# Kernel tuning notes

Measured on AMD Instinct MI355X. Metric: run time of the kernel, lower is better.

Reference implementation:

```python
import jax, jax.numpy as jnp
import numpy as np

N_NODES = 100000
N_EDGES = 1600000
NEG_SLOPE = 0.2
EPS = 1e-6


def setup_inputs() -> dict:
    key = jax.random.key(0)
    ks = jax.random.split(key, 14)
    s = 0.1  # weight init scale
    return {
        "x": jax.random.normal(ks[0], (N_NODES, 64), jnp.float32),
        "src": jax.random.randint(ks[1], (N_EDGES,), 0, N_NODES, jnp.int32),
        "dst": jax.random.randint(ks[2], (N_EDGES,), 0, N_NODES, jnp.int32),
        "W0": s * jax.random.normal(ks[3], (64, 128), jnp.float32),
        "al0": s * jax.random.normal(ks[4], (4, 32), jnp.float32),
        "ar0": s * jax.random.normal(ks[5], (4, 32), jnp.float32),
        "W1": s * jax.random.normal(ks[6], (128, 128), jnp.float32),
        "al1": s * jax.random.normal(ks[7], (4, 32), jnp.float32),
        "ar1": s * jax.random.normal(ks[8], (4, 32), jnp.float32),
        "resW1": s * jax.random.normal(ks[9], (128, 128), jnp.float32),
        "W2": s * jax.random.normal(ks[10], (128, 32), jnp.float32),
        "al2": s * jax.random.normal(ks[11], (1, 32), jnp.float32),
        "ar2": s * jax.random.normal(ks[12], (1, 32), jnp.float32),
        "resW2": s * jax.random.normal(ks[13], (128, 32), jnp.float32),
    }


def gat_conv(h, src, dst, W, al, ar, resW):
    """DGL-style GATConv. h: [N, Fin]; returns [N, H, D]."""
    H, D = al.shape
    feat = (h @ W).reshape(-1, H, D)                       # [N,H,D]
    el = jnp.sum(feat * al, axis=-1)                       # [N,H]
    er = jnp.sum(feat * ar, axis=-1)                       # [N,H]
    e = jax.nn.leaky_relu(el[src] + er[dst], NEG_SLOPE)    # [E,H]
    # segment softmax over destination nodes
    m = jax.ops.segment_max(e, dst, num_segments=N_NODES)  # [N,H]
    ex = jnp.exp(e - m[dst])                               # [E,H]
    denom = jax.ops.segment_sum(ex, dst, num_segments=N_NODES)
    alpha = ex / denom[dst]                                # [E,H]
    msg = alpha[:, :, None] * feat[src]                    # [E,H,D]
    rst = jax.ops.segment_sum(msg, dst, num_segments=N_NODES)  # [N,H,D]
    if resW is not None:
        rst = rst + (h @ resW).reshape(-1, H, D)
    return rst


def pairnorm_scs(x, scale=1.0):
    # 'PN-SCS' mode: scale-individually then center by original column mean
    col_mean = jnp.mean(x, axis=0)
    rownorm = jnp.sqrt(EPS + jnp.sum(x * x, axis=1, keepdims=True))
    return scale * x / rownorm - col_mean


def reference(x, src, dst, W0, al0, ar0, W1, al1, ar1, resW1, W2, al2, ar2, resW2):
    # layer 0: no residual, activation applied outside
    h = gat_conv(x, src, dst, W0, al0, ar0, None)          # [N,4,32]
    h = jax.nn.elu(h.reshape(h.shape[0], -1))              # [N,128]
    h = pairnorm_scs(h)
    # middle layer: residual + internal ELU (DGL applies activation inside),
    # then the outer loop flattens and applies ELU again
    h = jax.nn.elu(gat_conv(h, src, dst, W1, al1, ar1, resW1))  # [N,4,32]
    h = jax.nn.elu(h.reshape(h.shape[0], -1))              # [N,128]
    h = pairnorm_scs(h)
    # final layer: residual, mean over heads
    h = gat_conv(h, src, dst, W2, al2, ar2, resW2)         # [N,1,32]
    h = jnp.mean(h, axis=1)                                # [N,32]
    # dgl.mean_nodes readout on a single graph -> mean over nodes
    return jnp.mean(h, axis=0)                             # [32]
```

## Files before the change

### kernel.cpp

```cpp
#include <hip/hip_runtime.h>


typedef __attribute__((ext_vector_type(8))) short s8v;
typedef __attribute__((ext_vector_type(4))) float f4v;
typedef __attribute__((ext_vector_type(2))) float f2v;
typedef __attribute__((ext_vector_type(2))) _Float16 h2;
typedef __attribute__((ext_vector_type(4))) _Float16 h4;

__device__ __forceinline__ unsigned short f2bf(float f) {
  unsigned int x = __float_as_uint(f);
  x += 0x7fffu + ((x >> 16) & 1u);
  return (unsigned short)(x >> 16);
}
__device__ __forceinline__ float bf2f(unsigned short u) {
  return __uint_as_float(((unsigned int)u) << 16);
}
__device__ __forceinline__ unsigned short f2h(float f) {
  _Float16 h = (_Float16)f;
  return __builtin_bit_cast(unsigned short, h);
}
__device__ __forceinline__ unsigned char f2fp8(float v) {
  return (unsigned char)(__builtin_amdgcn_cvt_pk_fp8_f32(v, v, 0, false) & 0xff);
}
__device__ __forceinline__ float lrelu(float x) { return fmaxf(x, 0.2f * x); }
__device__ __forceinline__ float elu1(float x) { return x > 0.f ? x : __expf(x) - 1.f; }

__device__ __forceinline__ void pack_one(const float* W, const float* al, const float* ar,
                                         const float* resW, unsigned short* out,
                                         int K, int M, int BF, int H, int RES0, int t) {
  int c = t / K, k = t - c * K;
  float v = 0.f;
  if (c < BF) {
    v = W[k * BF + c];
  } else if (c < BF + H) {
    int h = c - BF;
    float s = 0.f;
    for (int d = 0; d < 32; d++) s += W[k * BF + h * 32 + d] * al[h * 32 + d];
    v = s;
  } else if (c < BF + 2 * H) {
    int h = c - BF - H;
    float s = 0.f;
    for (int d = 0; d < 32; d++) s += W[k * BF + h * 32 + d] * ar[h * 32 + d];
    v = s;
  } else if (c >= RES0) {
    v = resW[k * (M - RES0) + (c - RES0)];
  }
  unsigned short hi = f2bf(v);
  out[c * K + k] = hi;
  out[M * K + c * K + k] = f2bf(v - bf2f(hi));
}

__global__ __launch_bounds__(256) void hist_pack_k(const int* __restrict__ dst,
                                                   int* __restrict__ bhist, int E, int NB, int chunk, int P2B,
                                                   const float* __restrict__ W0, const float* __restrict__ al0,
                                                   const float* __restrict__ ar0,
                                                   const float* __restrict__ W1, const float* __restrict__ al1,
                                                   const float* __restrict__ ar1, const float* __restrict__ resW1,
                                                   const float* __restrict__ W2, const float* __restrict__ al2,
                                                   const float* __restrict__ ar2, const float* __restrict__ resW2,
                                                   unsigned short* __restrict__ w0t, unsigned short* __restrict__ w1t,
                                                   unsigned short* __restrict__ w2t) {
  if ((int)blockIdx.x < P2B) {
    __shared__ int h[512];
    for (int b = threadIdx.x; b < NB; b += 256) h[b] = 0;
    __syncthreads();
    int e0 = blockIdx.x * chunk;
    int e1 = min(E, e0 + chunk);
    for (int e = e0 + threadIdx.x; e < e1; e += 256) atomicAdd(&h[dst[e] >> 8], 1);
    __syncthreads();
    for (int b = threadIdx.x; b < NB; b += 256)
      bhist[(size_t)b * P2B + blockIdx.x] = h[b];
  } else {
    const int n0 = 144 * 64, n1 = 272 * 128, n2 = 80 * 128;
    int t = ((int)blockIdx.x - P2B) * 256 + threadIdx.x;
    if (t < n0) {
      pack_one(W0, al0, ar0, nullptr, w0t, 64, 144, 128, 4, 144, t);
    } else if (t < n0 + n1) {
      pack_one(W1, al1, ar1, resW1, w1t, 128, 272, 128, 4, 144, t - n0);
    } else if (t < n0 + n1 + n2) {
      pack_one(W2, al2, ar2, resW2, w2t, 128, 80, 32, 1, 48, t - n0 - n1);
    }
  }
}

__global__ __launch_bounds__(256) void pscan1(int* __restrict__ arr, int* __restrict__ bsum, int Nn) {
  __shared__ int s[256];
  int t = threadIdx.x;
  int base = blockIdx.x * 1024 + t * 4;
  int v0 = (base + 0 < Nn) ? arr[base + 0] : 0;
  int v1 = (base + 1 < Nn) ? arr[base + 1] : 0;
  int v2 = (base + 2 < Nn) ? arr[base + 2] : 0;
  int v3 = (base + 3 < Nn) ? arr[base + 3] : 0;
  s[t] = v0 + v1 + v2 + v3;
  __syncthreads();
  for (int off = 1; off < 256; off <<= 1) {
    int xv = (t >= off) ? s[t - off] : 0;
    __syncthreads();
    s[t] += xv;
    __syncthreads();
  }
  int excl = t ? s[t - 1] : 0;
  if (t == 255) bsum[blockIdx.x] = s[255];
  if (base + 0 < Nn) { arr[base + 0] = excl; excl += v0; }
  if (base + 1 < Nn) { arr[base + 1] = excl; excl += v1; }
  if (base + 2 < Nn) { arr[base + 2] = excl; excl += v2; }
  if (base + 3 < Nn) { arr[base + 3] = excl; }
}

__global__ __launch_bounds__(256) void pscan2(int* __restrict__ arr, const int* __restrict__ bsum,
                                              int Nn, int nb) {
  __shared__ int s[256];
  int t = threadIdx.x;
  s[t] = (t < nb) ? bsum[t] : 0;
  __syncthreads();
  for (int off = 1; off < 256; off <<= 1) {
    int xv = (t >= off) ? s[t - off] : 0;
    __syncthreads();
    s[t] += xv;
    __syncthreads();
  }
  int bb = blockIdx.x;
  int pref = bb ? s[bb - 1] : 0;
  if (pref != 0) {
    int base = bb * 1024 + t * 4;
    if (base + 0 < Nn) arr[base + 0] += pref;
    if (base + 1 < Nn) arr[base + 1] += pref;
    if (base + 2 < Nn) arr[base + 2] += pref;
    if (base + 3 < Nn) arr[base + 3] += pref;
  }
}

__global__ __launch_bounds__(256) void bscatter_k(const int* __restrict__ src, const int* __restrict__ dst,
                                                  const int* __restrict__ seg, unsigned int* __restrict__ ebuf,
                                                  int E, int NB, int chunk) {
  __shared__ int cur[512];
  for (int b = threadIdx.x; b < NB; b += 256)
    cur[b] = seg[(size_t)b * gridDim.x + blockIdx.x];
  __syncthreads();
  int e0 = blockIdx.x * chunk;
  int e1 = min(E, e0 + chunk);
  for (int e = e0 + threadIdx.x; e < e1; e += 256) {
    int d = dst[e];
    int pos = atomicAdd(&cur[d >> 8], 1);
    ebuf[pos] = ((unsigned int)src[e] << 8) | (unsigned int)(d & 255);
  }
}

__global__ __launch_bounds__(256) void fscatter_k(const unsigned int* __restrict__ ebuf,
                                                  const int* __restrict__ seg,
                                                  int* __restrict__ csr_src,
                                                  int* __restrict__ counts, int* __restrict__ rsp,
                                                  int E, int NB, int P2B, int Nn) {
  __shared__ int cnt[256];
  __shared__ int sc[256];
  __shared__ int cur[256];
  int b = blockIdx.x;
  int t = threadIdx.x;
  cnt[t] = 0;
  __syncthreads();
  int bstart = seg[(size_t)b * P2B];
  int bend = (b + 1 < NB) ? seg[(size_t)(b + 1) * P2B] : E;
  for (int e = bstart + t; e < bend; e += 256)
    atomicAdd(&cnt[ebuf[e] & 255u], 1);
  __syncthreads();
  int v = cnt[t];
  sc[t] = v;
  __syncthreads();
  for (int off = 1; off < 256; off <<= 1) {
    int xv = (t >= off) ? sc[t - off] : 0;
    __syncthreads();
    sc[t] += xv;
    __syncthreads();
  }
  int base = bstart + (t ? sc[t - 1] : 0);
  int node = (b << 8) + t;
  if (node < Nn) { counts[node] = v; rsp[node] = base; }
  cur[t] = base;
  __syncthreads();
  for (int e = bstart + t; e < bend; e += 256) {
    unsigned int sd = ebuf[e];
    int pos = atomicAdd(&cur[sd & 255u], 1);
    csr_src[pos] = (int)(sd >> 8);
  }
}

__global__ __launch_bounds__(256) void cmw_k(const float* __restrict__ colsum,
                                             const unsigned short* __restrict__ wt,
                                             float* __restrict__ cmw, int K, int M, float invN) {
  int c = blockIdx.x * 256 + threadIdx.x;
  if (c >= M) return;
  float s = 0.f;
  for (int k = 0; k < K; k++)
    s += colsum[k] * (bf2f(wt[c * K + k]) + bf2f(wt[(size_t)M * K + c * K + k]));
  cmw[c] = s * invN;
}

template <int K, int M, int R, int BF, int H, int RES0, bool AF32, bool CMW>
__global__ __launch_bounds__(256) void gemm_bf16(const void* __restrict__ Av,
                                                 const unsigned short* __restrict__ Bt,
                                                 const float* __restrict__ cmw,
                                                 unsigned char* __restrict__ feat8,
                                                 float* __restrict__ el, float* __restrict__ er,
                                                 unsigned short* __restrict__ resh, int nRowTiles) {
  constexpr int NT = M / 16;
  constexpr int PLANE = 16 * K * 2;
  constexpr int RS = (K == 128) ? 8 : 7;
  __shared__ unsigned char bbuf[2 * PLANE];
  int t = threadIdx.x;
  int w = t >> 6;
  int lane = t & 63;
  int tile0 = (int)blockIdx.x * (4 * R) + w * R;
  int r = lane & 15, q = lane >> 4;

  s8v afrag[R][K / 32];
  bool valid[R];
#pragma unroll
  for (int rr = 0; rr < R; rr++) {
    valid[rr] = (tile0 + rr) < nRowTiles;
    if (valid[rr]) {
      if constexpr (AF32) {
        const float* arow = (const float*)Av + (size_t)((tile0 + rr) * 16 + r) * K + q * 8;
#pragma unroll
        for (int kk = 0; kk < K / 32; kk++) {
          s8v v;
#pragma unroll
          for (int j = 0; j < 8; j++) v[j] = (short)f2bf(arow[kk * 32 + j]);
          afrag[rr][kk] = v;
        }
      } else {
        const unsigned short* arow = (const unsigned short*)Av + (size_t)((tile0 + rr) * 16 + r) * K + q * 8;
#pragma unroll
        for (int kk = 0; kk < K / 32; kk++) afrag[rr][kk] = *(const s8v*)(arow + kk * 32);
      }
    }
  }

  const unsigned char* gBhi = (const unsigned char*)Bt;
  const unsigned char* gBlo = (const unsigned char*)Bt + (size_t)M * K * 2;

  uint4 rh = {0, 0, 0, 0}, rl = {0, 0, 0, 0};
  if constexpr (K == 128) {
    rh = *(const uint4*)(gBhi + (size_t)0 * PLANE + t * 16);
    rl = *(const uint4*)(gBlo + (size_t)0 * PLANE + t * 16);
  } else {
    if (t < 128) rh = *(const uint4*)(gBhi + t * 16);
    else         rl = *(const uint4*)(gBlo + (t - 128) * 16);
  }

  for (int ct = 0; ct < NT; ct++) {
    if constexpr (K == 128) {
      unsigned x = (unsigned)t * 16;
      unsigned d = x ^ (((x >> RS) & 7u) << 4);
      *(uint4*)(bbuf + d) = rh;
      *(uint4*)(bbuf + PLANE + d) = rl;
    } else {
      if (t < 128) {
        unsigned x = (unsigned)t * 16;
        unsigned d = x ^ (((x >> RS) & 7u) << 4);
        *(uint4*)(bbuf + d) = rh;
      } else {
        unsigned x = (unsigned)(t - 128) * 16;
        unsigned d = x ^ (((x >> RS) & 7u) << 4);
        *(uint4*)(bbuf + PLANE + d) = rl;
      }
    }
    __syncthreads();
    if (ct + 1 < NT) {
      if constexpr (K == 128) {
        rh = *(const uint4*)(gBhi + (size_t)(ct + 1) * PLANE + t * 16);
        rl = *(const uint4*)(gBlo + (size_t)(ct + 1) * PLANE + t * 16);
      } else {
        if (t < 128) rh = *(const uint4*)(gBhi + (size_t)(ct + 1) * PLANE + t * 16);
        else         rl = *(const uint4*)(gBlo + (size_t)(ct + 1) * PLANE + (t - 128) * 16);
      }
    }
    s8v bhi[K / 32], blo[K / 32];
#pragma unroll
    for (int kk = 0; kk < K / 32; kk++) {
      unsigned off = (unsigned)(q * 16 + kk * 64);
      unsigned ad = ((unsigned)r << RS) + (off ^ (((unsigned)(r & 7)) << 4));
      bhi[kk] = *(const s8v*)(bbuf + ad);
      blo[kk] = *(const s8v*)(bbuf + PLANE + ad);
    }
    int col = ct * 16 + r;
    float cmwv = 0.f;
    if constexpr (CMW) cmwv = cmw[col];
#pragma unroll
    for (int rr = 0; rr < R; rr++) {
      if (!valid[rr]) continue;
      f4v acc = {0.f, 0.f, 0.f, 0.f};
#pragma unroll
      for (int kk = 0; kk < K / 32; kk++) {
        acc = __builtin_amdgcn_mfma_f32_16x16x32_bf16(afrag[rr][kk], bhi[kk], acc, 0, 0, 0);
        acc = __builtin_amdgcn_mfma_f32_16x16x32_bf16(afrag[rr][kk], blo[kk], acc, 0, 0, 0);
      }
      int row0 = (tile0 + rr) * 16 + q * 4;
#pragma unroll
      for (int i = 0; i < 4; i++) {
        float v = acc[i] - cmwv;
        size_t row = (size_t)(row0 + i);
        if (col < BF) {
          feat8[row * BF + col] = f2fp8(v);
        } else if (col < BF + H) {
          el[row * H + (col - BF)] = v;
        } else if (col < BF + 2 * H) {
          er[row * H + (col - BF - H)] = v;
        } else if (RES0 < M && col >= RES0) {
          resh[row * (M - RES0) + (col - RES0)] = f2h(v);
        }
      }
    }
    __syncthreads();
  }
}

template <int MODE>
__global__ __launch_bounds__(256) void aggregate4(const unsigned char* __restrict__ feat8,
                                                  const float* __restrict__ el4,
                                                  const float* __restrict__ er4,
                                                  const int* __restrict__ csr_src,
                                                  const int* __restrict__ rsp,
                                                  const int* __restrict__ counts,
                                                  const unsigned short* __restrict__ resh,
                                                  unsigned short* __restrict__ vbf,
                                                  float* __restrict__ rnrm, int Nn) {
  int n = (int)((blockIdx.x * blockDim.x + threadIdx.x) >> 6);
  if (n >= Nn) return;
  int lane = threadIdx.x & 63;
  int start = __builtin_amdgcn_readfirstlane(rsp[n]);
  int deg = __builtin_amdgcn_readfirstlane(counts[n]);
  int chunks = (deg + 15) >> 4;
  int slot = lane >> 2, h = lane & 3;
  float ern = er4[(size_t)n * 4 + h];
  int hl = lane >> 4;
  unsigned dby = (unsigned)lane << 1;
  f2v a01 = {0.f, 0.f};
  float dsum = 0.f;
  float elv = el4[(size_t)csr_src[start + slot] * 4 + h];
  for (int c = 0; c < chunks; c++) {
    const int* csp = csr_src + start + (c << 4);
    int sj[16];
#pragma unroll
    for (int j = 0; j < 16; j++) sj[j] = csp[j];
    float e = elv + ern;
    float exv = (((c << 4) + slot) < deg) ? __expf(fmaxf(e, 0.2f * e)) : 0.f;
    dsum += exv;
    if (c + 1 < chunks) elv = el4[(size_t)csp[16 + slot] * 4 + h];
#pragma unroll
    for (int j = 0; j < 16; j++) {
      float aw = __shfl(exv, (j << 2) | hl);
      unsigned short u = *(const unsigned short*)(feat8 + (((unsigned)sj[j] << 7) + dby));
      f2v fv = __builtin_amdgcn_cvt_pk_f32_fp8((int)u, false);
      f2v aw2 = {aw, aw};
      a01 = __builtin_elementwise_fma(fv, aw2, a01);
    }
  }
#pragma unroll
  for (int off = 4; off < 64; off <<= 1) dsum += __shfl_xor(dsum, off);
  float inv = dsum > 0.f ? 1.f / dsum : 0.f;
  float invh = __shfl(inv, hl);
  float v0, v1;
  if (MODE == 1) {
    h2 rr = *(const h2*)(resh + (size_t)n * 128 + lane * 2);
    v0 = elu1(elu1(a01[0] * invh + (float)rr[0]));
    v1 = elu1(elu1(a01[1] * invh + (float)rr[1]));
  } else {
    v0 = elu1(a01[0] * invh);
    v1 = elu1(a01[1] * invh);
  }
  float ss = v0 * v0 + v1 * v1;
#pragma unroll
  for (int off = 1; off < 64; off <<= 1) ss += __shfl_xor(ss, off);
  float rn = sqrtf(1e-6f + ss);
  float ri = 1.f / rn;
  unsigned int pk = (unsigned int)f2bf(v0 * ri) | ((unsigned int)f2bf(v1 * ri) << 16);
  *(unsigned int*)((char*)vbf + ((size_t)n << 8) + (lane << 2)) = pk;
  if (lane == 0) rnrm[n] = rn;
}

__global__ __launch_bounds__(256) void aggregate1(const unsigned char* __restrict__ feat8,
                                                  const float* __restrict__ el1,
                                                  const float* __restrict__ er1,
                                                  const int* __restrict__ csr_src,
                                                  const int* __restrict__ rsp,
                                                  const int* __restrict__ counts,
                                                  const unsigned short* __restrict__ res2h,
                                                  float* __restrict__ out2, int Nn) {
  int n = (int)((blockIdx.x * blockDim.x + threadIdx.x) >> 6);
  if (n >= Nn) return;
  int lane = threadIdx.x & 63;
  int start = __builtin_amdgcn_readfirstlane(rsp[n]);
  int deg = __builtin_amdgcn_readfirstlane(counts[n]);
  int chunks = (deg + 15) >> 4;
  int l16 = lane & 15;
  float ern = er1[n];
  int g = lane >> 3;
  unsigned dofs4 = (unsigned)(lane & 7) << 2;
  f2v acc01 = {0.f, 0.f}, acc23 = {0.f, 0.f};
  float dsum = 0.f;
  int sA = csr_src[start + l16];
  float elv = el1[sA];
  for (int c = 0; c < chunks; c++) {
    const int* csp = csr_src + start + (c << 4);
    float exv = (((c << 4) + l16) < deg) ? __expf(lrelu(elv + ern)) : 0.f;
    dsum += exv;
    int sAc = sA;
    if (c + 1 < chunks) {
      sA = csp[16 + l16];
      elv = el1[sA];
    }
#pragma unroll
    for (int t = 0; t < 2; t++) {
      int j = (t << 3) + g;
      int sj = __shfl(sAc, j);
      float aw = __shfl(exv, j);
      f2v aw2 = {aw, aw};
      unsigned int u = *(const unsigned int*)(feat8 + (((unsigned)sj << 5) + dofs4));
      f2v fa = __builtin_amdgcn_cvt_pk_f32_fp8((int)u, false);
      f2v fb = __builtin_amdgcn_cvt_pk_f32_fp8((int)u, true);
      acc01 = __builtin_elementwise_fma(fa, aw2, acc01);
      acc23 = __builtin_elementwise_fma(fb, aw2, acc23);
    }
  }
#pragma unroll
  for (int off = 1; off < 16; off <<= 1) dsum += __shfl_xor(dsum, off);
  float inv = dsum > 0.f ? 1.f / dsum : 0.f;
#pragma unroll
  for (int off = 8; off < 64; off <<= 1) {
    acc01[0] += __shfl_xor(acc01[0], off);
    acc01[1] += __shfl_xor(acc01[1], off);
    acc23[0] += __shfl_xor(acc23[0], off);
    acc23[1] += __shfl_xor(acc23[1], off);
  }
  if (lane < 8) {
    h4 rr = *(const h4*)(res2h + (size_t)n * 32 + (lane << 2));
    float4 o;
    o.x = acc01[0] * inv + (float)rr[0];
    o.y = acc01[1] * inv + (float)rr[1];
    o.z = acc23[0] * inv + (float)rr[2];
    o.w = acc23[1] * inv + (float)rr[3];
    *(float4*)(out2 + (size_t)n * 32 + (lane << 2)) = o;
  }
}

__global__ __launch_bounds__(256) void colsum_k(const unsigned short* __restrict__ vbf,
                                                const float* __restrict__ rnrm,
                                                float* __restrict__ colsum, int Nn) {
  __shared__ float ls[256];
  int tid = threadIdx.x;
  int c = tid & 127, rsub = tid >> 7;
  float cs = 0.f;
  for (int r = blockIdx.x * 2 + rsub; r < Nn; r += gridDim.x * 2)
    cs += bf2f(vbf[(size_t)r * 128 + c]) * rnrm[r];
  ls[tid] = cs;
  __syncthreads();
  if (tid < 128) atomicAdd(&colsum[tid], ls[tid] + ls[tid + 128]);
}

__global__ __launch_bounds__(256) void final_reduce(const float* __restrict__ out2,
                                                    float* __restrict__ outsum, int Nn) {
  __shared__ float ls[32];
  if (threadIdx.x < 32) ls[threadIdx.x] = 0.f;
  __syncthreads();
  int d = threadIdx.x & 31, rl = threadIdx.x >> 5;
  float acc = 0.f;
  for (int n = blockIdx.x * 8 + rl; n < Nn; n += gridDim.x * 8)
    acc += out2[(size_t)n * 32 + d];
  atomicAdd(&ls[d], acc);
  __syncthreads();
  if (threadIdx.x < 32) atomicAdd(&outsum[threadIdx.x], ls[threadIdx.x]);
}

__global__ void finalize_k(const float* __restrict__ outsum, float* __restrict__ out, float invN) {
  int t = threadIdx.x;
  if (t < 32) out[t] = outsum[t] * invN;
}

extern "C" void kernel_launch(void* const* d_in, const int* in_sizes, int n_in,
                              void* d_out, int out_size, void* d_ws, size_t ws_size,
                              hipStream_t stream) {
  const float* x     = (const float*)d_in[0];
  const int*   src   = (const int*)d_in[1];
  const int*   dst   = (const int*)d_in[2];
  const float* W0    = (const float*)d_in[3];
  const float* al0   = (const float*)d_in[4];
  const float* ar0   = (const float*)d_in[5];
  const float* W1    = (const float*)d_in[6];
  const float* al1   = (const float*)d_in[7];
  const float* ar1   = (const float*)d_in[8];
  const float* resW1 = (const float*)d_in[9];
  const float* W2    = (const float*)d_in[10];
  const float* al2   = (const float*)d_in[11];
  const float* ar2   = (const float*)d_in[12];
  const float* resW2 = (const float*)d_in[13];
  const int N = in_sizes[0] / 64;
  const int E = in_sizes[1];
  const float invN = 1.f / (float)N;
  const int Emax = E + 64;
  const int NB = (N + 255) >> 8;
  const int P2B = 512;
  const int chunk = (E + P2B - 1) / P2B;
  const int segN = NB * P2B;
  const int nbB = (segN + 1023) / 1024;

  char* p = (char*)d_ws;
  auto alloc = [&](size_t bytes) { char* r = p; p += (bytes + 255) & ~(size_t)255; return r; };

  char* zbase = p;
  float* colsumA = (float*)alloc(512);
  float* colsumB = (float*)alloc(512);
  float* outsum  = (float*)alloc(128);
  size_t zbytes = (size_t)(p - zbase);

  int* counts = (int*)alloc((size_t)4 * N);
  int* rsp    = (int*)alloc((size_t)4 * N);
  int* bsumB  = (int*)alloc(1024);
  int* bhist  = (int*)alloc((size_t)4 * segN);
  unsigned int* ebuf = (unsigned int*)alloc((size_t)4 * E);
  int* csr_src = (int*)alloc((size_t)4 * Emax);
  unsigned char*  feat8 = (unsigned char*)alloc((size_t)N * 128);
  unsigned short* vbf   = (unsigned short*)alloc((size_t)2 * N * 128);
  unsigned short* resh  = (unsigned short*)alloc((size_t)2 * N * 128);
  unsigned short* w0t = (unsigned short*)alloc((size_t)2 * 2 * 144 * 64);
  unsigned short* w1t = (unsigned short*)alloc((size_t)2 * 2 * 272 * 128);
  unsigned short* w2t = (unsigned short*)alloc((size_t)2 * 2 * 80 * 128);
  float* el4  = (float*)alloc((size_t)16 * N);
  float* er4  = (float*)alloc((size_t)16 * N);
  float* rnrm = (float*)alloc((size_t)4 * N);
  float* cmw1 = (float*)alloc(4 * 272);
  float* cmw2 = (float*)alloc(4 * 80);
  float* out2 = (float*)alloc((size_t)4 * N * 32);

  hipMemsetAsync(zbase, 0, zbytes, stream);
  hipMemsetAsync(csr_src + E, 0, (size_t)4 * (Emax - E), stream);

  const int packTot = 144 * 64 + 272 * 128 + 80 * 128;
  const int packBlocks = (packTot + 255) / 256;
  hist_pack_k<<<P2B + packBlocks, 256, 0, stream>>>(dst, bhist, E, NB, chunk, P2B,
                                                    W0, al0, ar0, W1, al1, ar1, resW1,
                                                    W2, al2, ar2, resW2, w0t, w1t, w2t);
  pscan1<<<nbB, 256, 0, stream>>>(bhist, bsumB, segN);
  pscan2<<<nbB, 256, 0, stream>>>(bhist, bsumB, segN, nbB);
  bscatter_k<<<P2B, 256, 0, stream>>>(src, dst, bhist, ebuf, E, NB, chunk);
  fscatter_k<<<NB, 256, 0, stream>>>(ebuf, bhist, csr_src, counts, rsp, E, NB, P2B, N);

  const int rowTiles = N / 16;
  const int gblocks = (rowTiles + 7) / 8;
  const int aggblocks = (N + 3) / 4;

  gemm_bf16<64, 144, 2, 128, 4, 144, true, false><<<gblocks, 256, 0, stream>>>(
      x, w0t, nullptr, feat8, el4, er4, nullptr, rowTiles);
  aggregate4<0><<<aggblocks, 256, 0, stream>>>(feat8, el4, er4, csr_src, rsp, counts, nullptr, vbf, rnrm, N);
  colsum_k<<<512, 256, 0, stream>>>(vbf, rnrm, colsumA, N);
  cmw_k<<<2, 256, 0, stream>>>(colsumA, w1t, cmw1, 128, 272, invN);

  gemm_bf16<128, 272, 2, 128, 4, 144, false, true><<<gblocks, 256, 0, stream>>>(
      vbf, w1t, cmw1, feat8, el4, er4, resh, rowTiles);
  aggregate4<1><<<aggblocks, 256, 0, stream>>>(feat8, el4, er4, csr_src, rsp, counts, resh, vbf, rnrm, N);
  colsum_k<<<512, 256, 0, stream>>>(vbf, rnrm, colsumB, N);
  cmw_k<<<1, 256, 0, stream>>>(colsumB, w2t, cmw2, 128, 80, invN);

  gemm_bf16<128, 80, 2, 32, 1, 48, false, true><<<gblocks, 256, 0, stream>>>(
      vbf, w2t, cmw2, feat8, el4, er4, resh, rowTiles);
  aggregate1<<<aggblocks, 256, 0, stream>>>(feat8, el4, er4, csr_src, rsp, counts, resh, out2, N);
  final_reduce<<<512, 256, 0, stream>>>(out2, outsum, N);
  finalize_k<<<1, 64, 0, stream>>>(outsum, (float*)d_out, invN);
}
```

Before: 488.8 us.

## Fuse scan fixup into scatter kernels, vectorize edge loads, prefetch CSR indices

Removes the pscan2 launch by having bscatter_k and fscatter_k each rescan the block sums in shared memory and add the prefix on the fly. The histogram and scatter kernels now read dst/src as int4 with the chunk size rounded to a multiple of four. The aggregation kernel software-prefetches the next chunk's CSR source indices into registers, and colsum reads two bf16 columns per thread. Together these aim to cut launch overhead and raise memory-access width, at the cost of redundant per-block scans and extra register pressure in the aggregation kernel.

```diff
diff --git a/kernel.cpp b/kernel.cpp
--- a/kernel.cpp
+++ b/kernel.cpp
@@ -66,7 +66,15 @@
     __syncthreads();
     int e0 = blockIdx.x * chunk;
     int e1 = min(E, e0 + chunk);
-    for (int e = e0 + threadIdx.x; e < e1; e += 256) atomicAdd(&h[dst[e] >> 8], 1);
+    int e = e0 + threadIdx.x * 4;
+    for (; e + 3 < e1; e += 1024) {
+      int4 d4 = *(const int4*)(dst + e);
+      atomicAdd(&h[d4.x >> 8], 1);
+      atomicAdd(&h[d4.y >> 8], 1);
+      atomicAdd(&h[d4.z >> 8], 1);
+      atomicAdd(&h[d4.w >> 8], 1);
+    }
+    for (; e < e1; e++) atomicAdd(&h[dst[e] >> 8], 1);
     __syncthreads();
     for (int b = threadIdx.x; b < NB; b += 256)
       bhist[(size_t)b * P2B + blockIdx.x] = h[b];
@@ -107,39 +115,43 @@
   if (base + 3 < Nn) { arr[base + 3] = excl; }
 }
 
-__global__ __launch_bounds__(256) void pscan2(int* __restrict__ arr, const int* __restrict__ bsum,
-                                              int Nn, int nb) {
-  __shared__ int s[256];
+__global__ __launch_bounds__(256) void bscatter_k(const int* __restrict__ src, const int* __restrict__ dst,
+                                                  const int* __restrict__ bhist, const int* __restrict__ bsumB,
+                                                  unsigned int* __restrict__ ebuf,
+                                                  int E, int NB, int chunk, int nbB) {
+  __shared__ int pref[256];
+  __shared__ int cur[512];
   int t = threadIdx.x;
-  s[t] = (t < nb) ? bsum[t] : 0;
+  pref[t] = (t < nbB) ? bsumB[t] : 0;
   __syncthreads();
   for (int off = 1; off < 256; off <<= 1) {
-    int xv = (t >= off) ? s[t - off] : 0;
-    __syncthreads();
-    s[t] += xv;
-    __syncthreads();
-  }
-  int bb = blockIdx.x;
-  int pref = bb ? s[bb - 1] : 0;
-  if (pref != 0) {
-    int base = bb * 1024 + t * 4;
-    if (base + 0 < Nn) arr[base + 0] += pref;
-    if (base + 1 < Nn) arr[base + 1] += pref;
-    if (base + 2 < Nn) arr[base + 2] += pref;
-    if (base + 3 < Nn) arr[base + 3] += pref;
-  }
-}
-
-__global__ __launch_bounds__(256) void bscatter_k(const int* __restrict__ src, const int* __restrict__ dst,
-                                                  const int* __restrict__ seg, unsigned int* __restrict__ ebuf,
-                                                  int E, int NB, int chunk) {
-  __shared__ int cur[512];
-  for (int b = threadIdx.x; b < NB; b += 256)
-    cur[b] = seg[(size_t)b * gridDim.x + blockIdx.x];
+    int xv = (t >= off) ? pref[t - off] : 0;
+    __syncthreads();
+    pref[t] += xv;
+    __syncthreads();
+  }
+  for (int b = t; b < NB; b += 256) {
+    size_t idx = (size_t)b * gridDim.x + blockIdx.x;
+    int sb = (int)(idx >> 10);
+    cur[b] = bhist[idx] + (sb ? pref[sb - 1] : 0);
+  }
   __syncthreads();
   int e0 = blockIdx.x * chunk;
   int e1 = min(E, e0 + chunk);
-  for (int e = e0 + threadIdx.x; e < e1; e += 256) {
+  int e = e0 + t * 4;
+  for (; e + 3 < e1; e += 1024) {
+    int4 d4 = *(const int4*)(dst + e);
+    int4 s4 = *(const int4*)(src + e);
+    int p0 = atomicAdd(&cur[d4.x >> 8], 1);
+    ebuf[p0] = ((unsigned int)s4.x << 8) | (unsigned int)(d4.x & 255);
+    int p1 = atomicAdd(&cur[d4.y >> 8], 1);
+    ebuf[p1] = ((unsigned int)s4.y << 8) | (unsigned int)(d4.y & 255);
+    int p2 = atomicAdd(&cur[d4.z >> 8], 1);
+    ebuf[p2] = ((unsigned int)s4.z << 8) | (unsigned int)(d4.z & 255);
+    int p3 = atomicAdd(&cur[d4.w >> 8], 1);
+    ebuf[p3] = ((unsigned int)s4.w << 8) | (unsigned int)(d4.w & 255);
+  }
+  for (; e < e1; e++) {
     int d = dst[e];
     int pos = atomicAdd(&cur[d >> 8], 1);
     ebuf[pos] = ((unsigned int)src[e] << 8) | (unsigned int)(d & 255);
@@ -147,19 +159,34 @@
 }
 
 __global__ __launch_bounds__(256) void fscatter_k(const unsigned int* __restrict__ ebuf,
-                                                  const int* __restrict__ seg,
+                                                  const int* __restrict__ bhist, const int* __restrict__ bsumB,
                                                   int* __restrict__ csr_src,
                                                   int* __restrict__ counts, int* __restrict__ rsp,
-                                                  int E, int NB, int P2B, int Nn) {
+                                                  int E, int NB, int P2B, int Nn, int nbB) {
+  __shared__ int pref[256];
   __shared__ int cnt[256];
   __shared__ int sc[256];
   __shared__ int cur[256];
   int b = blockIdx.x;
   int t = threadIdx.x;
+  pref[t] = (t < nbB) ? bsumB[t] : 0;
   cnt[t] = 0;
   __syncthreads();
-  int bstart = seg[(size_t)b * P2B];
-  int bend = (b + 1 < NB) ? seg[(size_t)(b + 1) * P2B] : E;
+  for (int off = 1; off < 256; off <<= 1) {
+    int xv = (t >= off) ? pref[t - off] : 0;
+    __syncthreads();
+    pref[t] += xv;
+    __syncthreads();
+  }
+  size_t i1 = (size_t)b * P2B;
+  int sb1 = (int)(i1 >> 10);
+  int bstart = bhist[i1] + (sb1 ? pref[sb1 - 1] : 0);
+  int bend = E;
+  if (b + 1 < NB) {
+    size_t i2 = (size_t)(b + 1) * P2B;
+    int sb2 = (int)(i2 >> 10);
+    bend = bhist[i2] + (sb2 ? pref[sb2 - 1] : 0);
+  }
   for (int e = bstart + t; e < bend; e += 256)
     atomicAdd(&cnt[ebuf[e] & 255u], 1);
   __syncthreads();
@@ -336,16 +363,23 @@
   unsigned dby = (unsigned)lane << 1;
   f2v a01 = {0.f, 0.f};
   float dsum = 0.f;
-  float elv = el4[(size_t)csr_src[start + slot] * 4 + h];
+  const int* csp0 = csr_src + start;
+  int sj[16];
+#pragma unroll
+  for (int j = 0; j < 16; j++) sj[j] = csp0[j];
+  float elv = el4[(size_t)csp0[slot] * 4 + h];
   for (int c = 0; c < chunks; c++) {
-    const int* csp = csr_src + start + (c << 4);
-    int sj[16];
-#pragma unroll
-    for (int j = 0; j < 16; j++) sj[j] = csp[j];
     float e = elv + ern;
     float exv = (((c << 4) + slot) < deg) ? __expf(fmaxf(e, 0.2f * e)) : 0.f;
     dsum += exv;
-    if (c + 1 < chunks) elv = el4[(size_t)csp[16 + slot] * 4 + h];
+    int sjn[16];
+    bool more = (c + 1 < chunks);
+    if (more) {
+      const int* csp1 = csr_src + start + ((c + 1) << 4);
+#pragma unroll
+      for (int j = 0; j < 16; j++) sjn[j] = csp1[j];
+      elv = el4[(size_t)csp1[slot] * 4 + h];
+    }
 #pragma unroll
     for (int j = 0; j < 16; j++) {
       float aw = __shfl(exv, (j << 2) | hl);
@@ -353,6 +387,10 @@
       f2v fv = __builtin_amdgcn_cvt_pk_f32_fp8((int)u, false);
       f2v aw2 = {aw, aw};
       a01 = __builtin_elementwise_fma(fv, aw2, a01);
+    }
+    if (more) {
+#pragma unroll
+      for (int j = 0; j < 16; j++) sj[j] = sjn[j];
     }
   }
 #pragma unroll
@@ -446,15 +484,24 @@
 __global__ __launch_bounds__(256) void colsum_k(const unsigned short* __restrict__ vbf,
                                                 const float* __restrict__ rnrm,
                                                 float* __restrict__ colsum, int Nn) {
-  __shared__ float ls[256];
+  __shared__ float2 ls[256];
   int tid = threadIdx.x;
-  int c = tid & 127, rsub = tid >> 7;
-  float cs = 0.f;
-  for (int r = blockIdx.x * 2 + rsub; r < Nn; r += gridDim.x * 2)
-    cs += bf2f(vbf[(size_t)r * 128 + c]) * rnrm[r];
+  int c2 = tid & 63;
+  int rsub = tid >> 6;
+  float2 cs = {0.f, 0.f};
+  for (int r = blockIdx.x * 4 + rsub; r < Nn; r += gridDim.x * 4) {
+    unsigned u = *(const unsigned*)(vbf + (size_t)r * 128 + c2 * 2);
+    float rn = rnrm[r];
+    cs.x += bf2f((unsigned short)(u & 0xffffu)) * rn;
+    cs.y += bf2f((unsigned short)(u >> 16)) * rn;
+  }
   ls[tid] = cs;
   __syncthreads();
-  if (tid < 128) atomicAdd(&colsum[tid], ls[tid] + ls[tid + 128]);
+  if (tid < 64) {
+    float2 a = ls[tid], b = ls[tid + 64], c = ls[tid + 128], d = ls[tid + 192];
+    atomicAdd(&colsum[2 * tid], a.x + b.x + c.x + d.x);
+    atomicAdd(&colsum[2 * tid + 1], a.y + b.y + c.y + d.y);
+  }
 }
 
 __global__ __launch_bounds__(256) void final_reduce(const float* __restrict__ out2,
@@ -499,7 +546,7 @@
   const int Emax = E + 64;
   const int NB = (N + 255) >> 8;
   const int P2B = 512;
-  const int chunk = (E + P2B - 1) / P2B;
+  const int chunk = (((E + P2B - 1) / P2B) + 3) & ~3;
   const int segN = NB * P2B;
   const int nbB = (segN + 1023) / 1024;
 
@@ -540,9 +587,8 @@
                                                     W0, al0, ar0, W1, al1, ar1, resW1,
                                                     W2, al2, ar2, resW2, w0t, w1t, w2t);
   pscan1<<<nbB, 256, 0, stream>>>(bhist, bsumB, segN);
-  pscan2<<<nbB, 256, 0, stream>>>(bhist, bsumB, segN, nbB);
-  bscatter_k<<<P2B, 256, 0, stream>>>(src, dst, bhist, ebuf, E, NB, chunk);
-  fscatter_k<<<NB, 256, 0, stream>>>(ebuf, bhist, csr_src, counts, rsp, E, NB, P2B, N);
+  bscatter_k<<<P2B, 256, 0, stream>>>(src, dst, bhist, bsumB, ebuf, E, NB, chunk, nbB);
+  fscatter_k<<<NB, 256, 0, stream>>>(ebuf, bhist, bsumB, csr_src, counts, rsp, E, NB, P2B, N, nbB);
 
   const int rowTiles = N / 16;
   const int gblocks = (rowTiles + 7) / 8;
```

After: 476.6 us. 2.5% less time.
